# Kernel tuning notes

Measured on AMD Instinct MI355X. Metric: run time of the kernel, lower is better.

## Reference

```python
import jax, jax.numpy as jnp
import numpy as np

VOC_SIZE = 50000
WORD_DIM = 64
CPR_DIM = 64
NUM_RELS = 7
BATCH = 1024
N_LEAVES = 64  # complete binary tree, depth 6
BOUND = 0.05


def setup_inputs() -> dict:
    key = jax.random.key(0)
    ks = jax.random.split(key, 16)
    u = lambda k, shape: jax.random.uniform(k, shape, jnp.float32, -BOUND, BOUND)
    return {
        "left_leaves": jax.random.randint(ks[0], (BATCH, N_LEAVES), 0, VOC_SIZE),
        "right_leaves": jax.random.randint(ks[1], (BATCH, N_LEAVES), 0, VOC_SIZE),
        "voc_w": u(ks[2], (WORD_DIM, VOC_SIZE)),
        "voc_b": u(ks[3], (WORD_DIM,)),
        "cps_w": u(ks[4], (WORD_DIM, 2 * WORD_DIM)),
        "cps_b": u(ks[5], (WORD_DIM,)),
        "cpst_w": u(ks[6], (WORD_DIM, WORD_DIM * WORD_DIM)),
        "cpst_b": u(ks[7], (WORD_DIM,)),
        "cpr_w": u(ks[8], (CPR_DIM, 2 * WORD_DIM)),
        "cpr_b": u(ks[9], (CPR_DIM,)),
        "cprt_w": u(ks[10], (CPR_DIM, WORD_DIM * WORD_DIM)),
        "cprt_b": u(ks[11], (CPR_DIM,)),
        "sm_w": u(ks[12], (NUM_RELS, CPR_DIM)),
        "sm_b": u(ks[13], (NUM_RELS,)),
    }


def _compose(x, cps_w, cps_b, cpst_w, cpst_b):
    # x: [B, N, d] leaf embeddings of a complete binary tree; reduce level by level.
    B, N, d = x.shape
    while N > 1:
        L = x[:, 0::2, :]  # [B, N/2, d]
        R = x[:, 1::2, :]
        cps = jnp.einsum("bnf,ef->bne", jnp.concatenate([L, R], axis=-1), cps_w) + cps_b
        # NOTE: source computes ger(left, left) for interior nodes (left with itself)
        kron = (L[:, :, :, None] * L[:, :, None, :]).reshape(B, N // 2, d * d)
        cps_t = jnp.einsum("bnk,ek->bne", kron, cpst_w) + cpst_b
        x = jnp.tanh(cps + cps_t)
        N //= 2
    return x[:, 0, :]  # [B, d]


def reference(left_leaves, right_leaves, voc_w, voc_b, cps_w, cps_b, cpst_w, cpst_b,
              cpr_w, cpr_b, cprt_w, cprt_b, sm_w, sm_b):
    # onehot @ Linear == embedding gather of columns of voc_w, plus bias
    left_emb = voc_w.T[left_leaves] + voc_b    # [B, N, d]
    right_emb = voc_w.T[right_leaves] + voc_b
    l = _compose(left_emb, cps_w, cps_b, cpst_w, cpst_b)   # [B, d]
    r = _compose(right_emb, cps_w, cps_b, cpst_w, cpst_b)  # [B, d]
    cpr = jnp.concatenate([l, r], axis=-1) @ cpr_w.T + cpr_b
    kron = (l[:, :, None] * r[:, None, :]).reshape(l.shape[0], -1)  # [B, d*d]
    cpr_t = kron @ cprt_w.T + cprt_b
    act = jax.nn.leaky_relu(cpr + cpr_t, negative_slope=0.01)
    logits = act @ sm_w.T + sm_b
    return jax.nn.softmax(logits, axis=-1)  # [B, num_rels]
```

## Files before the change

kernel.cpp:

```cpp
#include <hip/hip_runtime.h>
#include <hip/hip_bf16.h>
#include <cstdint>
#include <cstddef>

typedef _Float16 f16x8 __attribute__((ext_vector_type(8)));
typedef float    f32x4 __attribute__((ext_vector_type(4)));

#define VOC    50000
#define W2T    2432
#define NSTG_T 19
#define W2F    4224
#define NSTG_F 33
#define STG    8192
#define XSTR   72
#define TPW    8
#define IPW    16

__device__ __attribute__((aligned(256))) unsigned short g_vocT[(size_t)VOC * 64];
__device__ __attribute__((aligned(256))) unsigned short g_roots[2048 * 64];
__device__ __attribute__((aligned(256))) unsigned short g_cpstU[(size_t)NSTG_T * STG];
__device__ __attribute__((aligned(256))) unsigned short g_cprtU[(size_t)NSTG_F * STG];
__device__ float g_smw[7 * 64];
__device__ float g_smb[7];
__device__ float g_biasC[64];
__device__ float g_biasF[64];

#define KE(BI0,BJ0,R0,BI1,BJ1,R1) \
    ((BI0) | ((BJ0) << 3) | ((R0) << 6) | ((BI1) << 7) | ((BJ1) << 10) | ((R1) << 13))
__device__ __constant__ int g_ktab[18] = {
    KE(0,0,1, 0,1,1), KE(0,2,0, 0,3,0), KE(0,4,0, 0,5,0), KE(0,6,0, 0,7,0),
    KE(1,1,1, 1,2,1), KE(1,3,0, 1,4,0), KE(1,5,0, 1,6,0), KE(1,7,0, 2,2,1),
    KE(2,3,1, 2,4,0), KE(2,5,0, 2,6,0), KE(2,7,0, 3,3,1), KE(3,4,1, 3,5,0),
    KE(3,6,0, 3,7,0), KE(4,4,1, 4,5,1), KE(4,6,0, 4,7,0), KE(5,5,1, 5,6,1),
    KE(5,7,0, 6,6,1), KE(6,7,1, 7,7,1)
};

__device__ __forceinline__ float b2f(unsigned short u) {
    unsigned int x = ((unsigned int)u) << 16;
    return __builtin_bit_cast(float, x);
}
__device__ __forceinline__ unsigned short f2b(float f) {
    return __builtin_bit_cast(unsigned short, (__bf16)f);
}
__device__ __forceinline__ unsigned short f2h(float f) {
    return __builtin_bit_cast(unsigned short, (_Float16)f);
}
__device__ __forceinline__ float scrub(float v) {
    return fminf(fmaxf(v, -64.f), 64.f);
}
__device__ __forceinline__ float ldf(const void* p, size_t i, int isb) {
    return isb ? b2f(((const unsigned short*)p)[i]) : ((const float*)p)[i];
}
__device__ __forceinline__ int detect_isb(const void* voc_b) {
    const unsigned int* p = (const unsigned int*)voc_b;
    int ok = 1;
    for (int k = 0; k < 32; k++) {
        float v = b2f((unsigned short)(p[k] & 0xFFFFu));
        if (!(fabsf(v) <= 0.0502f)) ok = 0;
    }
    return ok;
}

__global__ __launch_bounds__(256) void k_prep(
    const void* voc_w, const void* voc_b,
    const void* cps_w, const void* cps_b, const void* cpst_w, const void* cpst_b,
    const void* cpr_w, const void* cpr_b, const void* cprt_w, const void* cprt_b,
    const void* sm_w, const void* sm_b)
{
    __shared__ float tile[64][65];
    __shared__ float vb[64];
    const int isb = detect_isb(voc_b);
    if (blockIdx.x < 512) {
        int gid = blockIdx.x * 256 + threadIdx.x;
        int stride = 512 * 256;
        for (int d = gid; d < 64 * W2T; d += stride) {
            int s    = d / STG;
            int rem  = d - s * STG;
            int kbl  = rem >> 11;
            int rem2 = rem & 2047;
            int nt   = rem2 >> 9;
            int rem3 = rem2 & 511;
            int q    = rem3 >> 7;
            int rem4 = rem3 & 127;
            int sub  = rem4 >> 3;
            int z    = rem4 & 7;
            int n    = nt * 16 + sub;
            int k    = s * 128 + kbl * 32 + q * 8 + z;
            float w;
            if (k < 2304) {
                int b   = k >> 6;
                int p2l = (k >> 5) & 1;
                int bi = 0, remb = b;
                while (remb >= 8 - bi) { remb -= 8 - bi; bi++; }
                int bj = bi + remb;
                int i = bi * 8 + z;
                int j = bj * 8 + 2 * q + p2l;
                w = ldf(cpst_w, (size_t)n * 4096 + i * 64 + j, isb);
                if (bi != bj)
                    w += ldf(cpst_w, (size_t)n * 4096 + j * 64 + i, isb);
            } else {
                w = ldf(cps_w, (size_t)n * 128 + (k - 2304), isb);
            }
            g_cpstU[d] = f2h(w);
        }
        for (int d = gid; d < 64 * W2F; d += stride) {
            int s    = d / STG;
            int rem  = d - s * STG;
            int kbl  = rem >> 11;
            int rem2 = rem & 2047;
            int nt   = rem2 >> 9;
            int rem3 = rem2 & 511;
            int q    = rem3 >> 7;
            int rem4 = rem3 & 127;
            int sub  = rem4 >> 3;
            int z    = rem4 & 7;
            int n    = nt * 16 + sub;
            int k    = s * 128 + kbl * 32 + q * 8 + z;
            float v2 = (k < 4096) ? ldf(cprt_w, (size_t)n * 4096 + k, isb)
                                  : ldf(cpr_w,  (size_t)n * 128 + (k - 4096), isb);
            g_cprtU[d] = f2h(v2);
        }
        for (int i = gid; i < 448; i += stride) g_smw[i] = ldf(sm_w, i, isb);
        if (gid < 64) {
            g_biasC[gid] = ldf(cps_b, gid, isb) + ldf(cpst_b, gid, isb);
            g_biasF[gid] = ldf(cpr_b, gid, isb) + ldf(cprt_b, gid, isb);
        }
        if (gid < 7) g_smb[gid] = ldf(sm_b, gid, isb);
    } else {
        int t = threadIdx.x;
        if (t < 64) vb[t] = ldf(voc_b, t, isb);
        int v0 = (blockIdx.x - 512) * 64;
        int vl = t & 63, dr = t >> 6;
        #pragma unroll
        for (int i = 0; i < 16; i++) {
            int d = dr * 16 + i;
            int v = v0 + vl;
            tile[vl][d] = (v < VOC) ? ldf(voc_w, (size_t)d * VOC + v, isb) : 0.f;
        }
        __syncthreads();
        int dl = t & 63, vr0 = t >> 6;
        #pragma unroll
        for (int i = 0; i < 16; i++) {
            int vr = vr0 * 16 + i;
            int v = v0 + vr;
            if (v < VOC) g_vocT[(size_t)v * 64 + dl] = f2h(tile[vr][dl] + vb[dl]);
        }
    }
}

#define EPILOGUE(CO)                                                          \
    if (lv < 5) {                                                             \
        _Pragma("unroll")                                                     \
        for (int nt = 0; nt < 4; nt++) {                                      \
            int e = nt * 16 + sub;                                            \
            _Pragma("unroll")                                                 \
            for (int rr = 0; rr < 4; rr++) {                                  \
                int m = chv[CO] * 16 + q * 4 + rr;                            \
                if (m < nodes) {                                              \
                    int t2 = m >> lg, n2 = m & (cnew - 1);                    \
                    Xs[(t2 * 64 + n2) * XSTR + e] =                           \
                        f2h(tanhf(scrub(acc[CO][nt][rr] + biasC[e])));        \
                }                                                             \
            }                                                                 \
        }                                                                     \
    } else {                                                                  \
        _Pragma("unroll")                                                     \
        for (int nt = 0; nt < 4; nt++) {                                      \
            int e = nt * 16 + sub;                                            \
            _Pragma("unroll")                                                 \
            for (int rr = 0; rr < 4; rr++) {                                  \
                int m = q * 4 + rr;                                           \
                if (m < TPW)                                                  \
                    g_roots[((size_t)wg * TPW + m) * 64 + e] =                \
                        f2h(tanhf(scrub(acc[CO][nt][rr] + biasC[e])));        \
            }                                                                 \
        }                                                                     \
    }

#define EXSEND(CS)                                                            \
    { _Pragma("unroll")                                                       \
      for (int nt = 0; nt < 4; nt++)                                          \
          *(f32x4*)(exchS + wave * 1024 + nt * 256 + lane * 4) = acc[CS][nt]; }

#define EXRECV(CO)                                                            \
    { _Pragma("unroll")                                                       \
      for (int nt = 0; nt < 4; nt++) {                                        \
          f32x4 v_ = *(const f32x4*)(exchS + (wave ^ 1) * 1024 + nt * 256 + lane * 4); \
          _Pragma("unroll")                                                   \
          for (int z = 0; z < 4; z++) acc[CO][nt][z] += v_[z];                \
      } }

#define BLD8(BF, SBASE)                                                       \
    { const unsigned short* gs_ = (SBASE) + half * 4096 + lane * 8;           \
      _Pragma("unroll")                                                       \
      for (int j = 0; j < 8; j++)                                             \
          BF[j] = *(const f16x8*)(gs_ + (j >> 2) * 2048 + (j & 3) * 512); }

#define KMM(CI, AV, B0, B1, B2, B3)                                           \
    { f16x8 a_ = (AV);                                                        \
      acc[CI][0] = __builtin_amdgcn_mfma_f32_16x16x32_f16(a_, B0, acc[CI][0], 0, 0, 0); \
      acc[CI][1] = __builtin_amdgcn_mfma_f32_16x16x32_f16(a_, B1, acc[CI][1], 0, 0, 0); \
      acc[CI][2] = __builtin_amdgcn_mfma_f32_16x16x32_f16(a_, B2, acc[CI][2], 0, 0, 0); \
      acc[CI][3] = __builtin_amdgcn_mfma_f32_16x16x32_f16(a_, B3, acc[CI][3], 0, 0, 0); }

#define KBLOCKR(BF, BI, BJ, RLD)                                              \
    if (act[0]) {                                                             \
        if (RLD) {                                                            \
            lA0 = *(const f16x8*)(Xs + slotL[0] + (BI) * 8);                  \
            if (act[1]) lA1 = *(const f16x8*)(Xs + slotL[1] + (BI) * 8);      \
            if (act[2]) lA2 = *(const f16x8*)(Xs + slotL[2] + (BI) * 8);      \
            if (act[3]) lA3 = *(const f16x8*)(Xs + slotL[3] + (BI) * 8);      \
        }                                                                     \
        _Float16 sc0[4], sc1[4];                                              \
        _Pragma("unroll")                                                     \
        for (int c = 0; c < 4; c++)                                           \
            if (act[c]) {                                                     \
                unsigned pr_ = *(const unsigned*)(Xs + slotL[c] + (BJ) * 8 + 2 * q); \
                sc0[c] = __builtin_bit_cast(_Float16, (unsigned short)(pr_ & 0xFFFFu)); \
                sc1[c] = __builtin_bit_cast(_Float16, (unsigned short)(pr_ >> 16));     \
            }                                                                 \
        _Pragma("unroll")                                                     \
        for (int p2 = 0; p2 < 2; p2++) {                                      \
            KMM(0, lA0 * (p2 ? sc1[0] : sc0[0]),                              \
                BF[p2 * 4 + 0], BF[p2 * 4 + 1], BF[p2 * 4 + 2], BF[p2 * 4 + 3]) \
            if (act[1]) KMM(1, lA1 * (p2 ? sc1[1] : sc0[1]),                  \
                BF[p2 * 4 + 0], BF[p2 * 4 + 1], BF[p2 * 4 + 2], BF[p2 * 4 + 3]) \
            if (act[2]) KMM(2, lA2 * (p2 ? sc1[2] : sc0[2]),                  \
                BF[p2 * 4 + 0], BF[p2 * 4 + 1], BF[p2 * 4 + 2], BF[p2 * 4 + 3]) \
            if (act[3]) KMM(3, lA3 * (p2 ? sc1[3] : sc0[3]),                  \
                BF[p2 * 4 + 0], BF[p2 * 4 + 1], BF[p2 * 4 + 2], BF[p2 * 4 + 3]) \
        }                                                                     \
    }

#define KRUNR(S, BF)                                                          \
    {                                                                         \
        int e_   = g_ktab[S];                                                 \
        int ent_ = half ? (e_ >> 7) : e_;                                     \
        int bi_  = ent_ & 7;                                                  \
        int bj_  = (ent_ >> 3) & 7;                                           \
        int rld_ = (ent_ >> 6) & 1;                                           \
        KBLOCKR((BF), bi_, bj_, rld_)                                         \
    }

__global__ __launch_bounds__(512, 2)
void k_tree(const int* __restrict__ lleaf, const int* __restrict__ rleaf)
{
    __shared__ __attribute__((aligned(16))) unsigned short Xs[512 * XSTR];
    __shared__ __attribute__((aligned(16))) float exchS[8192];
    __shared__ float biasC[64];
    const int tid = threadIdx.x;
    const int wg  = blockIdx.x;

    if (tid < 64) biasC[tid] = g_biasC[tid];

    {
        int t = tid >> 6, i = tid & 63;
        int gidx = wg * TPW + t;
        int b = (gidx < 1024) ? gidx : gidx - 1024;
        const int* lv2 = (gidx < 1024) ? lleaf : rleaf;
        int idx = lv2[b * 64 + i];
        idx = (idx < 0) ? 0 : ((idx >= VOC) ? VOC - 1 : idx);
        const uint4* src = (const uint4*)(g_vocT + (size_t)idx * 64);
        uint4* dst = (uint4*)(Xs + tid * XSTR);
        #pragma unroll
        for (int z = 0; z < 8; z++) dst[z] = src[z];
    }

    __syncthreads();

    const int lane = tid & 63, wave = tid >> 6;
    const int q = lane >> 4, sub = lane & 15;
    const int p = wave >> 1, half = wave & 1;

    #pragma unroll 1
    for (int lv = 0; lv < 6; lv++) {
        const int lg = 5 - lv;
        const int cnew = 1 << lg;
        const int nodes = TPW << lg;
        const int nchunks = (nodes + 15) >> 4;

        int act[4], chv[4], slotL[4];
        #pragma unroll
        for (int c = 0; c < 4; c++) {
            int ch = p + 4 * c;
            act[c] = (ch < nchunks);
            chv[c] = ch;
            int m = ch * 16 + sub;
            if (!act[c] || m >= nodes) m = 0;
            int t = m >> lg, n = m & (cnew - 1);
            slotL[c] = (t * 64 + 2 * n) * XSTR;
        }

        f16x8 lA0 = {}, lA1 = {}, lA2 = {}, lA3 = {};
        f32x4 acc[4][4];
        #pragma unroll
        for (int c = 0; c < 4; c++)
            #pragma unroll
            for (int nt = 0; nt < 4; nt++)
                #pragma unroll
                for (int z = 0; z < 4; z++) acc[c][nt][z] = 0.f;

        f16x8 bfA[8], bfB[8];
        if (act[0]) BLD8(bfA, g_cpstU)
        #pragma unroll 1
        for (int t = 0; t < 9; t++) {
            if (act[0]) BLD8(bfB, g_cpstU + (size_t)(2 * t + 1) * STG)
            KRUNR(2 * t, bfA)
            if (act[0]) BLD8(bfA, g_cpstU + (size_t)(2 * t + 2) * STG)
            KRUNR(2 * t + 1, bfB)
        }

        if (act[0]) {
            #pragma unroll
            for (int p2 = 0; p2 < 2; p2++) {
                #pragma unroll
                for (int c = 0; c < 4; c++) {
                    if (!act[c]) continue;
                    f16x8 A = *(const f16x8*)(Xs + slotL[c] + half * XSTR + p2 * 32 + q * 8);
                    acc[c][0] = __builtin_amdgcn_mfma_f32_16x16x32_f16(A, bfA[p2 * 4 + 0], acc[c][0], 0, 0, 0);
                    acc[c][1] = __builtin_amdgcn_mfma_f32_16x16x32_f16(A, bfA[p2 * 4 + 1], acc[c][1], 0, 0, 0);
                    acc[c][2] = __builtin_amdgcn_mfma_f32_16x16x32_f16(A, bfA[p2 * 4 + 2], acc[c][2], 0, 0, 0);
                    acc[c][3] = __builtin_amdgcn_mfma_f32_16x16x32_f16(A, bfA[p2 * 4 + 3], acc[c][3], 0, 0, 0);
                }
            }
        }

        if (half == 0) { if (act[1]) EXSEND(1) } else { if (act[0]) EXSEND(0) }
        __syncthreads();
        if (half == 0) {
            if (act[0]) { EXRECV(0) EPILOGUE(0) }
        } else {
            if (act[1]) { EXRECV(1) EPILOGUE(1) }
        }
        __syncthreads();
        if (half == 0) { if (act[3]) EXSEND(3) } else { if (act[2]) EXSEND(2) }
        __syncthreads();
        if (half == 0) {
            if (act[2]) { EXRECV(2) EPILOGUE(2) }
        } else {
            if (act[3]) { EXRECV(3) EPILOGUE(3) }
        }
        __syncthreads();
    }
}

#define BLD4(BF, S)                                                           \
    { const unsigned short* gs_ = g_cprtU + (size_t)(S) * STG + w * 512 + lane * 8; \
      _Pragma("unroll")                                                       \
      for (int j = 0; j < 4; j++)                                             \
          BF[j] = *(const f16x8*)(gs_ + j * 2048); }

#define FKRONR(S, BF)                                                         \
    { _Pragma("unroll")                                                       \
      for (int ii = 0; ii < 2; ii++) {                                        \
          int i_ = 2 * (S) + ii;                                              \
          _Float16 li_ = __builtin_bit_cast(_Float16, Lv[rowLo + i_]);        \
          _Pragma("unroll")                                                   \
          for (int p2 = 0; p2 < 2; p2++) {                                    \
              f16x8 afr_ = Ra[p2] * li_;                                      \
              acc = __builtin_amdgcn_mfma_f32_16x16x32_f16(afr_, BF[2 * ii + p2], acc, 0, 0, 0); \
          }                                                                   \
      } }

__global__ __launch_bounds__(256, 2) void k_final(const void* __restrict__ voc_b,
                                                  void* __restrict__ out)
{
    __shared__ __attribute__((aligned(16))) unsigned short Lv[IPW * XSTR], Rv[IPW * XSTR];
    __shared__ float actS[IPW][65];
    __shared__ float smw[7][64];
    __shared__ float smbS[7];
    __shared__ float biasF[64];
    const int tid = threadIdx.x, wg = blockIdx.x;
    const int isb = detect_isb(voc_b);

    if (tid < 64) biasF[tid] = g_biasF[tid];
    if (tid < 7)  smbS[tid] = g_smb[tid];
    for (int z = tid; z < 448; z += 256) smw[z >> 6][z & 63] = g_smw[z];

    {
        int side = tid >> 7, idx = tid & 127;
        int item = idx >> 3, piece = idx & 7;
        const uint4* s4 = (const uint4*)(g_roots +
            ((size_t)(side * 1024) + (size_t)wg * IPW + item) * 64 + piece * 8);
        uint4* d4 = (uint4*)((side ? Rv : Lv) + item * XSTR + piece * 8);
        *d4 = *s4;
    }

    const int lane = tid & 63, w = tid >> 6;
    const int q = lane >> 4, sub = lane & 15;
    const int rowLo = sub * XSTR;

    f16x8 bA[4], bB[4];
    BLD4(bA, 0)

    __syncthreads();

    f16x8 Ra[2];
    Ra[0] = *(const f16x8*)(Rv + rowLo + q * 8);
    Ra[1] = *(const f16x8*)(Rv + rowLo + 32 + q * 8);

    f32x4 acc;
    #pragma unroll
    for (int z = 0; z < 4; z++) acc[z] = 0.f;

    #pragma unroll 1
    for (int t = 0; t < 16; t++) {
        BLD4(bB, 2 * t + 1)
        FKRONR(2 * t, bA)
        BLD4(bA, 2 * t + 2)
        FKRONR(2 * t + 1, bB)
    }

    {
        f16x8 A4[4];
        A4[0] = *(const f16x8*)(Lv + rowLo + q * 8);
        A4[1] = *(const f16x8*)(Lv + rowLo + 32 + q * 8);
        A4[2] = *(const f16x8*)(Rv + rowLo + q * 8);
        A4[3] = *(const f16x8*)(Rv + rowLo + 32 + q * 8);
        #pragma unroll
        for (int kbl = 0; kbl < 4; kbl++)
            acc = __builtin_amdgcn_mfma_f32_16x16x32_f16(A4[kbl], bA[kbl], acc, 0, 0, 0);
    }

    {
        int e = w * 16 + sub;
        #pragma unroll
        for (int rr = 0; rr < 4; rr++) {
            int item = q * 4 + rr;
            float v = scrub(acc[rr] + biasF[e]);
            v = (v > 0.f) ? v : 0.01f * v;
            actS[item][e] = v;
        }
    }
    __syncthreads();

    if (tid < IPW) {
        float lg[7];
        #pragma unroll
        for (int j = 0; j < 7; j++) lg[j] = smbS[j];
        for (int e = 0; e < 64; e++) {
            float a = actS[tid][e];
            #pragma unroll
            for (int j = 0; j < 7; j++) lg[j] += smw[j][e] * a;
        }
        float mx = lg[0];
        #pragma unroll
        for (int j = 1; j < 7; j++) mx = fmaxf(mx, lg[j]);
        float s = 0.f, pr[7];
        #pragma unroll
        for (int j = 0; j < 7; j++) { pr[j] = expf(lg[j] - mx); s += pr[j]; }
        float inv = 1.f / s;
        size_t b = (size_t)wg * IPW + tid;
        if (isb) {
            unsigned short* o = (unsigned short*)out;
            #pragma unroll
            for (int j = 0; j < 7; j++) o[b * 7 + j] = f2b(pr[j] * inv);
        } else {
            float* o = (float*)out;
            #pragma unroll
            for (int j = 0; j < 7; j++) o[b * 7 + j] = pr[j] * inv;
        }
    }
}

extern "C" void kernel_launch(void* const* d_in, const int* in_sizes, int n_in,
                              void* d_out, int out_size, void* d_ws, size_t ws_size,
                              hipStream_t stream) {
    const int* lleaf = (const int*)d_in[0];
    const int* rleaf = (const int*)d_in[1];
    const void* voc_w  = d_in[2];
    const void* voc_b  = d_in[3];
    const void* cps_w  = d_in[4];
    const void* cps_b  = d_in[5];
    const void* cpst_w = d_in[6];
    const void* cpst_b = d_in[7];
    const void* cpr_w  = d_in[8];
    const void* cpr_b  = d_in[9];
    const void* cprt_w = d_in[10];
    const void* cprt_b = d_in[11];
    const void* sm_w   = d_in[12];
    const void* sm_b   = d_in[13];

    k_prep<<<512 + (VOC + 63) / 64, 256, 0, stream>>>(
        voc_w, voc_b, cps_w, cps_b, cpst_w, cpst_b,
        cpr_w, cpr_b, cprt_w, cprt_b, sm_w, sm_b);
    k_tree<<<2048 / TPW, 512, 0, stream>>>(lleaf, rleaf);
    k_final<<<64, 256, 0, stream>>>(voc_b, (unsigned short*)d_out);
}
```

Measured before the change: 177.3 us.

## Redistribute small tree levels across waves by splitting output columns

```diff
diff --git a/kernel.cpp b/kernel.cpp
--- a/kernel.cpp
+++ b/kernel.cpp
@@ -149,7 +149,7 @@
 }
 
 #define EPILOGUE(CO)                                                          \
-    if (lv < 5) {                                                             \
+    {                                                                         \
         _Pragma("unroll")                                                     \
         for (int nt = 0; nt < 4; nt++) {                                      \
             int e = nt * 16 + sub;                                            \
@@ -161,18 +161,6 @@
                     Xs[(t2 * 64 + n2) * XSTR + e] =                           \
                         f2h(tanhf(scrub(acc[CO][nt][rr] + biasC[e])));        \
                 }                                                             \
-            }                                                                 \
-        }                                                                     \
-    } else {                                                                  \
-        _Pragma("unroll")                                                     \
-        for (int nt = 0; nt < 4; nt++) {                                      \
-            int e = nt * 16 + sub;                                            \
-            _Pragma("unroll")                                                 \
-            for (int rr = 0; rr < 4; rr++) {                                  \
-                int m = q * 4 + rr;                                           \
-                if (m < TPW)                                                  \
-                    g_roots[((size_t)wg * TPW + m) * 64 + e] =                \
-                        f2h(tanhf(scrub(acc[CO][nt][rr] + biasC[e])));        \
             }                                                                 \
         }                                                                     \
     }
@@ -242,6 +230,50 @@
         KBLOCKR((BF), bi_, bj_, rld_)                                         \
     }
 
+#define DBLD2(BF, SBASE)                                                      \
+    { const unsigned short* gs_ = (SBASE) + half * 4096 + lane * 8;           \
+      BF[0] = *(const f16x8*)(gs_ + (ntb + 0) * 512);                         \
+      BF[1] = *(const f16x8*)(gs_ + (ntb + 1) * 512);                         \
+      BF[2] = *(const f16x8*)(gs_ + 2048 + (ntb + 0) * 512);                  \
+      BF[3] = *(const f16x8*)(gs_ + 2048 + (ntb + 1) * 512); }
+
+#define DBLD1(BF, SBASE)                                                      \
+    { const unsigned short* gs_ = (SBASE) + half * 4096 + ntb * 512 + lane * 8; \
+      BF[0] = *(const f16x8*)(gs_);                                           \
+      BF[1] = *(const f16x8*)(gs_ + 2048); }
+
+#define DKRUN2(S, BF)                                                         \
+    {                                                                         \
+        int e_   = g_ktab[S];                                                 \
+        int ent_ = half ? (e_ >> 7) : e_;                                     \
+        int bi_  = ent_ & 7;                                                  \
+        int bj_  = (ent_ >> 3) & 7;                                           \
+        if ((ent_ >> 6) & 1) lAD = *(const f16x8*)(Xs + slotD + bi_ * 8);     \
+        unsigned pr_ = *(const unsigned*)(Xs + slotD + bj_ * 8 + 2 * q);      \
+        _Float16 s0_ = __builtin_bit_cast(_Float16, (unsigned short)(pr_ & 0xFFFFu)); \
+        _Float16 s1_ = __builtin_bit_cast(_Float16, (unsigned short)(pr_ >> 16));     \
+        f16x8 a0_ = lAD * s0_;                                                \
+        accD0 = __builtin_amdgcn_mfma_f32_16x16x32_f16(a0_, BF[0], accD0, 0, 0, 0); \
+        accD1 = __builtin_amdgcn_mfma_f32_16x16x32_f16(a0_, BF[1], accD1, 0, 0, 0); \
+        f16x8 a1_ = lAD * s1_;                                                \
+        accD0 = __builtin_amdgcn_mfma_f32_16x16x32_f16(a1_, BF[2], accD0, 0, 0, 0); \
+        accD1 = __builtin_amdgcn_mfma_f32_16x16x32_f16(a1_, BF[3], accD1, 0, 0, 0); \
+    }
+
+#define DKRUN1(S, BF)                                                         \
+    {                                                                         \
+        int e_   = g_ktab[S];                                                 \
+        int ent_ = half ? (e_ >> 7) : e_;                                     \
+        int bi_  = ent_ & 7;                                                  \
+        int bj_  = (ent_ >> 3) & 7;                                           \
+        if ((ent_ >> 6) & 1) lAD = *(const f16x8*)(Xs + slotD + bi_ * 8);     \
+        unsigned pr_ = *(const unsigned*)(Xs + slotD + bj_ * 8 + 2 * q);      \
+        _Float16 s0_ = __builtin_bit_cast(_Float16, (unsigned short)(pr_ & 0xFFFFu)); \
+        _Float16 s1_ = __builtin_bit_cast(_Float16, (unsigned short)(pr_ >> 16));     \
+        accD0 = __builtin_amdgcn_mfma_f32_16x16x32_f16(lAD * s0_, BF[0], accD0, 0, 0, 0); \
+        accD0 = __builtin_amdgcn_mfma_f32_16x16x32_f16(lAD * s1_, BF[1], accD0, 0, 0, 0); \
+    }
+
 __global__ __launch_bounds__(512, 2)
 void k_tree(const int* __restrict__ lleaf, const int* __restrict__ rleaf)
 {
@@ -279,68 +311,171 @@
         const int nodes = TPW << lg;
         const int nchunks = (nodes + 15) >> 4;
 
-        int act[4], chv[4], slotL[4];
-        #pragma unroll
-        for (int c = 0; c < 4; c++) {
-            int ch = p + 4 * c;
-            act[c] = (ch < nchunks);
-            chv[c] = ch;
-            int m = ch * 16 + sub;
-            if (!act[c] || m >= nodes) m = 0;
-            int t = m >> lg, n = m & (cnew - 1);
-            slotL[c] = (t * 64 + 2 * n) * XSTR;
-        }
-
-        f16x8 lA0 = {}, lA1 = {}, lA2 = {}, lA3 = {};
-        f32x4 acc[4][4];
-        #pragma unroll
-        for (int c = 0; c < 4; c++)
+        if (nchunks >= 4) {
+            int act[4], chv[4], slotL[4];
             #pragma unroll
-            for (int nt = 0; nt < 4; nt++)
+            for (int c = 0; c < 4; c++) {
+                int ch = p + 4 * c;
+                act[c] = (ch < nchunks);
+                chv[c] = ch;
+                int m = ch * 16 + sub;
+                if (!act[c] || m >= nodes) m = 0;
+                int t = m >> lg, n = m & (cnew - 1);
+                slotL[c] = (t * 64 + 2 * n) * XSTR;
+            }
+
+            f16x8 lA0 = {}, lA1 = {}, lA2 = {}, lA3 = {};
+            f32x4 acc[4][4];
+            #pragma unroll
+            for (int c = 0; c < 4; c++)
                 #pragma unroll
-                for (int z = 0; z < 4; z++) acc[c][nt][z] = 0.f;
-
-        f16x8 bfA[8], bfB[8];
-        if (act[0]) BLD8(bfA, g_cpstU)
-        #pragma unroll 1
-        for (int t = 0; t < 9; t++) {
-            if (act[0]) BLD8(bfB, g_cpstU + (size_t)(2 * t + 1) * STG)
-            KRUNR(2 * t, bfA)
-            if (act[0]) BLD8(bfA, g_cpstU + (size_t)(2 * t + 2) * STG)
-            KRUNR(2 * t + 1, bfB)
-        }
-
-        if (act[0]) {
-            #pragma unroll
-            for (int p2 = 0; p2 < 2; p2++) {
+                for (int nt = 0; nt < 4; nt++)
+                    #pragma unroll
+                    for (int z = 0; z < 4; z++) acc[c][nt][z] = 0.f;
+
+            f16x8 bfA[8], bfB[8];
+            if (act[0]) BLD8(bfA, g_cpstU)
+            #pragma unroll 1
+            for (int t = 0; t < 9; t++) {
+                if (act[0]) BLD8(bfB, g_cpstU + (size_t)(2 * t + 1) * STG)
+                KRUNR(2 * t, bfA)
+                if (act[0]) BLD8(bfA, g_cpstU + (size_t)(2 * t + 2) * STG)
+                KRUNR(2 * t + 1, bfB)
+            }
+            if (act[0]) {
                 #pragma unroll
-                for (int c = 0; c < 4; c++) {
-                    if (!act[c]) continue;
-                    f16x8 A = *(const f16x8*)(Xs + slotL[c] + half * XSTR + p2 * 32 + q * 8);
-                    acc[c][0] = __builtin_amdgcn_mfma_f32_16x16x32_f16(A, bfA[p2 * 4 + 0], acc[c][0], 0, 0, 0);
-                    acc[c][1] = __builtin_amdgcn_mfma_f32_16x16x32_f16(A, bfA[p2 * 4 + 1], acc[c][1], 0, 0, 0);
-                    acc[c][2] = __builtin_amdgcn_mfma_f32_16x16x32_f16(A, bfA[p2 * 4 + 2], acc[c][2], 0, 0, 0);
-                    acc[c][3] = __builtin_amdgcn_mfma_f32_16x16x32_f16(A, bfA[p2 * 4 + 3], acc[c][3], 0, 0, 0);
+                for (int p2 = 0; p2 < 2; p2++) {
+                    #pragma unroll
+                    for (int c = 0; c < 4; c++) {
+                        if (!act[c]) continue;
+                        f16x8 A = *(const f16x8*)(Xs + slotL[c] + half * XSTR + p2 * 32 + q * 8);
+                        acc[c][0] = __builtin_amdgcn_mfma_f32_16x16x32_f16(A, bfA[p2 * 4 + 0], acc[c][0], 0, 0, 0);
+                        acc[c][1] = __builtin_amdgcn_mfma_f32_16x16x32_f16(A, bfA[p2 * 4 + 1], acc[c][1], 0, 0, 0);
+                        acc[c][2] = __builtin_amdgcn_mfma_f32_16x16x32_f16(A, bfA[p2 * 4 + 2], acc[c][2], 0, 0, 0);
+                        acc[c][3] = __builtin_amdgcn_mfma_f32_16x16x32_f16(A, bfA[p2 * 4 + 3], acc[c][3], 0, 0, 0);
+                    }
                 }
             }
-        }
-
-        if (half == 0) { if (act[1]) EXSEND(1) } else { if (act[0]) EXSEND(0) }
-        __syncthreads();
-        if (half == 0) {
-            if (act[0]) { EXRECV(0) EPILOGUE(0) }
+
+            if (half == 0) { if (act[1]) EXSEND(1) } else { if (act[0]) EXSEND(0) }
+            __syncthreads();
+            if (half == 0) {
+                if (act[0]) { EXRECV(0) EPILOGUE(0) }
+            } else {
+                if (act[1]) { EXRECV(1) EPILOGUE(1) }
+            }
+            __syncthreads();
+            if (half == 0) { if (act[3]) EXSEND(3) } else { if (act[2]) EXSEND(2) }
+            __syncthreads();
+            if (half == 0) {
+                if (act[2]) { EXRECV(2) EPILOGUE(2) }
+            } else {
+                if (act[3]) { EXRECV(3) EPILOGUE(3) }
+            }
+            __syncthreads();
+        } else if (nchunks == 2) {
+            const int chD = p >> 1;
+            const int ntb = (p & 1) * 2;
+            int mD = chD * 16 + sub;
+            int tD = mD >> lg, nD = mD & (cnew - 1);
+            const int slotD = (tD * 64 + 2 * nD) * XSTR;
+            f16x8 lAD = {};
+            f32x4 accD0 = {0.f,0.f,0.f,0.f}, accD1 = {0.f,0.f,0.f,0.f};
+
+            f16x8 dA[4], dB[4];
+            DBLD2(dA, g_cpstU)
+            #pragma unroll 1
+            for (int t = 0; t < 9; t++) {
+                DBLD2(dB, g_cpstU + (size_t)(2 * t + 1) * STG)
+                DKRUN2(2 * t, dA)
+                DBLD2(dA, g_cpstU + (size_t)(2 * t + 2) * STG)
+                DKRUN2(2 * t + 1, dB)
+            }
+            {
+                #pragma unroll
+                for (int p2 = 0; p2 < 2; p2++) {
+                    f16x8 A = *(const f16x8*)(Xs + slotD + half * XSTR + p2 * 32 + q * 8);
+                    accD0 = __builtin_amdgcn_mfma_f32_16x16x32_f16(A, dA[p2 * 2 + 0], accD0, 0, 0, 0);
+                    accD1 = __builtin_amdgcn_mfma_f32_16x16x32_f16(A, dA[p2 * 2 + 1], accD1, 0, 0, 0);
+                }
+            }
+            if (half == 1) {
+                *(f32x4*)(exchS + p * 1024 + lane * 4) = accD0;
+                *(f32x4*)(exchS + p * 1024 + 256 + lane * 4) = accD1;
+            }
+            __syncthreads();
+            if (half == 0) {
+                {   f32x4 v0 = *(const f32x4*)(exchS + p * 1024 + lane * 4);
+                    f32x4 v1 = *(const f32x4*)(exchS + p * 1024 + 256 + lane * 4);
+                    #pragma unroll
+                    for (int z = 0; z < 4; z++) { accD0[z] += v0[z]; accD1[z] += v1[z]; }
+                }
+                #pragma unroll
+                for (int j = 0; j < 2; j++) {
+                    int e = (ntb + j) * 16 + sub;
+                    #pragma unroll
+                    for (int rr = 0; rr < 4; rr++) {
+                        int m = chD * 16 + q * 4 + rr;
+                        int t2 = m >> lg, n2 = m & (cnew - 1);
+                        float av = j ? accD1[rr] : accD0[rr];
+                        Xs[(t2 * 64 + n2) * XSTR + e] = f2h(tanhf(scrub(av + biasC[e])));
+                    }
+                }
+            }
+            __syncthreads();
         } else {
-            if (act[1]) { EXRECV(1) EPILOGUE(1) }
-        }
-        __syncthreads();
-        if (half == 0) { if (act[3]) EXSEND(3) } else { if (act[2]) EXSEND(2) }
-        __syncthreads();
-        if (half == 0) {
-            if (act[2]) { EXRECV(2) EPILOGUE(2) }
-        } else {
-            if (act[3]) { EXRECV(3) EPILOGUE(3) }
-        }
-        __syncthreads();
+            const int ntb = p;
+            int mD = sub;
+            if (mD >= nodes) mD = 0;
+            int tD = mD >> lg, nD = mD & (cnew - 1);
+            const int slotD = (tD * 64 + 2 * nD) * XSTR;
+            f16x8 lAD = {};
+            f32x4 accD0 = {0.f,0.f,0.f,0.f};
+
+            f16x8 dA[2], dB[2];
+            DBLD1(dA, g_cpstU)
+            #pragma unroll 1
+            for (int t = 0; t < 9; t++) {
+                DBLD1(dB, g_cpstU + (size_t)(2 * t + 1) * STG)
+                DKRUN1(2 * t, dA)
+                DBLD1(dA, g_cpstU + (size_t)(2 * t + 2) * STG)
+                DKRUN1(2 * t + 1, dB)
+            }
+            {
+                #pragma unroll
+                for (int p2 = 0; p2 < 2; p2++) {
+                    f16x8 A = *(const f16x8*)(Xs + slotD + half * XSTR + p2 * 32 + q * 8);
+                    accD0 = __builtin_amdgcn_mfma_f32_16x16x32_f16(A, dA[p2], accD0, 0, 0, 0);
+                }
+            }
+            if (half == 1)
+                *(f32x4*)(exchS + p * 1024 + lane * 4) = accD0;
+            __syncthreads();
+            if (half == 0) {
+                {   f32x4 v0 = *(const f32x4*)(exchS + p * 1024 + lane * 4);
+                    #pragma unroll
+                    for (int z = 0; z < 4; z++) accD0[z] += v0[z];
+                }
+                int e = ntb * 16 + sub;
+                if (lv < 5) {
+                    #pragma unroll
+                    for (int rr = 0; rr < 4; rr++) {
+                        int m = q * 4 + rr;
+                        int t2 = m >> lg, n2 = m & (cnew - 1);
+                        Xs[(t2 * 64 + n2) * XSTR + e] = f2h(tanhf(scrub(accD0[rr] + biasC[e])));
+                    }
+                } else {
+                    #pragma unroll
+                    for (int rr = 0; rr < 4; rr++) {
+                        int m = q * 4 + rr;
+                        if (m < TPW)
+                            g_roots[((size_t)wg * TPW + m) * 64 + e] =
+                                f2h(tanhf(scrub(accD0[rr] + biasC[e])));
+                    }
+                }
+            }
+            __syncthreads();
+        }
     }
 }
 
```

Result: faster. 165.6 us (median of 2 runs) (-6.6%).
